# Performance work log

Hardware: AMD Instinct MI355X
Metric: run time of the kernel (lower is better)

## Reference

```python
import jax, jax.numpy as jnp
import numpy as np

B, M, IN, H = 4096, 16, 512, 512


def _linear_params(key, out_dim, in_dim):
    kw, kb = jax.random.split(key)
    s = 1.0 / np.sqrt(in_dim)
    W = jax.random.uniform(kw, (out_dim, in_dim), jnp.float32, -s, s)
    b = jax.random.uniform(kb, (out_dim,), jnp.float32, -s, s)
    return W, b


def setup_inputs() -> dict:
    key = jax.random.key(0)
    ks = jax.random.split(key, 15)
    inp = {
        "input": jax.random.normal(ks[0], (B, IN), jnp.float32),
        "h0": jax.random.normal(ks[1], (B, H), jnp.float32),
        "c0": jax.random.normal(ks[2], (B, H), jnp.float32),
        "all_c_b_e_w": jax.random.normal(ks[3], (B, M, H), jnp.float32),
        "all_num_word": jax.random.randint(ks[4], (B,), 0, M + 1, jnp.int32),
    }
    names = ["ii", "hi", "if_", "hf", "ig", "hg", "io", "ho", "lx", "lc"]
    in_dims = [IN, H, IN, H, IN, H, IN, H, IN, H]
    for n, d, k in zip(names, in_dims, ks[5:15]):
        W, b = _linear_params(k, H, d)
        inp["W_" + n] = W
        inp["b_" + n] = b
    return inp


def _lin(x, W, b):
    return x @ W.T + b


def reference(input, h0, c0, all_c_b_e_w, all_num_word,
              W_ii, b_ii, W_hi, b_hi, W_if_, b_if_, W_hf, b_hf,
              W_ig, b_ig, W_hg, b_hg, W_io, b_io, W_ho, b_ho,
              W_lx, b_lx, W_lc, b_lc):
    i = jax.nn.sigmoid(_lin(input, W_ii, b_ii) + _lin(h0, W_hi, b_hi))   # [B,H]
    f = jax.nn.sigmoid(_lin(input, W_if_, b_if_) + _lin(h0, W_hf, b_hf))  # computed but unused, as in original
    g = jnp.tanh(_lin(input, W_ig, b_ig) + _lin(h0, W_hg, b_hg))         # [B,H]
    o = jax.nn.sigmoid(_lin(input, W_io, b_io) + _lin(h0, W_ho, b_ho))   # [B,H]

    # lattice word-cell gates, vectorized over the ragged word dim with a mask
    lx = _lin(input, W_lx, b_lx)                 # [B,H]
    lc = _lin(all_c_b_e_w, W_lc, b_lc)           # [B,M,H]
    i_b = jax.nn.sigmoid(lx[:, None, :] + lc)    # [B,M,H]
    mask = (jnp.arange(M)[None, :] < all_num_word[:, None])  # [B,M]
    exp_b = jnp.exp(i_b) * mask[:, :, None].astype(i_b.dtype)  # [B,M,H]
    exp_i = jnp.exp(i)                                         # [B,H]
    denom = exp_i + jnp.sum(exp_b, axis=1)                     # [B,H]
    c_words = jnp.sum((exp_b / denom[:, None, :]) * all_c_b_e_w, axis=1)
    c_lat = c_words + (exp_i / denom) * g
    c = jnp.where((all_num_word > 0)[:, None], c_lat, g)       # num_word==0 -> c=g
    h1 = o * jnp.tanh(c)
    return (h1, c)
```

## Files before the change

### kernel.cpp

```cpp
#include <hip/hip_runtime.h>
#include <hip/hip_bf16.h>
#include <stdint.h>


typedef __attribute__((ext_vector_type(8))) short short8;
typedef __attribute__((ext_vector_type(4))) float f32x4;
typedef __attribute__((ext_vector_type(4))) unsigned short us4;

__device__ __forceinline__ unsigned short f2bf(float f) {
  union { float f; unsigned u; } v; v.f = f;
  return (unsigned short)((v.u + 0x7fffu + ((v.u >> 16) & 1u)) >> 16);
}
__device__ __forceinline__ unsigned short f2bf_h(float f) {
  __hip_bfloat16 h = __float2bfloat16(f);
  return *reinterpret_cast<unsigned short*>(&h);
}
__device__ __forceinline__ float bf2f(unsigned short u) {
  return __uint_as_float((unsigned)u << 16);
}
__device__ __forceinline__ float sigmoidf_(float x) {
  return 1.f / (1.f + __expf(-x));
}
__device__ __forceinline__ float fast_tanh(float x) {
  float e = __expf(-2.f * fmaxf(x, -30.f));
  return (1.f - e) / (1.f + e);
}

__global__ void k_cvt_all(const float* __restrict__ x, const float* __restrict__ h,
                          const float* __restrict__ Wii, const float* __restrict__ Wig,
                          const float* __restrict__ Wio, const float* __restrict__ Wlx,
                          const float* __restrict__ Whi, const float* __restrict__ Whg,
                          const float* __restrict__ Who, const float* __restrict__ Wlcf,
                          unsigned short* __restrict__ XH, unsigned short* __restrict__ Wcat,
                          unsigned short* __restrict__ Wlc) {
  const int bb = blockIdx.x;
  const int tid = threadIdx.x;
  us4 o;
  if (bb < 4096) {
    const int t = bb * 256 + tid;
    const int b = t >> 8;
    const int col = (t & 255) * 4;
    const float* src = (col < 512) ? (x + (size_t)b * 512 + col)
                                   : (h + (size_t)b * 512 + (col - 512));
    f32x4 v = *(const f32x4*)src;
    o[0] = f2bf(v[0]); o[1] = f2bf(v[1]); o[2] = f2bf(v[2]); o[3] = f2bf(v[3]);
    *(us4*)(XH + (size_t)t * 4) = o;
  } else if (bb < 6144) {
    const int t = (bb - 4096) * 256 + tid;
    const int row = t >> 8;
    const int col = (t & 255) * 4;
    const int sec = row >> 9, r = row & 511;
    if (col < 512) {
      const float* W = sec == 0 ? Wii : sec == 1 ? Wig : sec == 2 ? Wio : Wlx;
      f32x4 v = *(const f32x4*)(W + (size_t)r * 512 + col);
      o[0] = f2bf(v[0]); o[1] = f2bf(v[1]); o[2] = f2bf(v[2]); o[3] = f2bf(v[3]);
    } else if (sec < 3) {
      const float* W = sec == 0 ? Whi : sec == 1 ? Whg : Who;
      f32x4 v = *(const f32x4*)(W + (size_t)r * 512 + (col - 512));
      o[0] = f2bf(v[0]); o[1] = f2bf(v[1]); o[2] = f2bf(v[2]); o[3] = f2bf(v[3]);
    } else {
      o[0] = 0; o[1] = 0; o[2] = 0; o[3] = 0;
    }
    *(us4*)(Wcat + (size_t)t * 4) = o;
  } else {
    const int t = (bb - 6144) * 256 + tid;
    f32x4 v = *(const f32x4*)(Wlcf + (size_t)t * 4);
    o[0] = f2bf(v[0]); o[1] = f2bf(v[1]); o[2] = f2bf(v[2]); o[3] = f2bf(v[3]);
    *(us4*)(Wlc + (size_t)t * 4) = o;
  }
}

__global__ __launch_bounds__(256) void k_gemm0(
    const unsigned short* __restrict__ A, const unsigned short* __restrict__ Bm,
    unsigned short* __restrict__ C, int Ndim, int Kdim, int nbx) {
  __shared__ unsigned short As[2][128 * 64];
  __shared__ unsigned short Bs[2][128 * 64];
  const int tid = threadIdx.x;
  const int lane = tid & 63, wid = tid >> 6;
  const int wr = wid >> 1, wc = wid & 1;
  const int l15 = lane & 15, lhi = lane >> 4;

  const int chunk = gridDim.x >> 3;
  const int bid = (blockIdx.x & 7) * chunk + (blockIdx.x >> 3);
  const int brow = bid / nbx, bcol = bid % nbx;
  const int m0 = brow * 128, n0 = bcol * 128;

  f32x4 acc[4][4];
#pragma unroll
  for (int i = 0; i < 4; ++i)
#pragma unroll
    for (int j = 0; j < 4; ++j) acc[i][j] = (f32x4){0.f, 0.f, 0.f, 0.f};

  const int cb0 = wid * 64;
  auto stage = [&](int buf, int k0) {
#pragma unroll
    for (int q = 0; q < 4; ++q) {
      const int cb = q * 256 + cb0;
      const int chunkid = cb + lane;
      const int row = chunkid >> 3, slot = chunkid & 7;
      const int kk = k0 + ((slot ^ (row & 7)) << 3);
      __builtin_amdgcn_global_load_lds(
          (const __attribute__((address_space(1))) unsigned int*)(A + (size_t)(m0 + row) * Kdim + kk),
          (__attribute__((address_space(3))) unsigned int*)(As[buf] + cb * 8), 16, 0, 0);
      __builtin_amdgcn_global_load_lds(
          (const __attribute__((address_space(1))) unsigned int*)(Bm + (size_t)(n0 + row) * Kdim + kk),
          (__attribute__((address_space(3))) unsigned int*)(Bs[buf] + cb * 8), 16, 0, 0);
    }
  };

  const int nt = Kdim >> 6;
  stage(0, 0);
  __syncthreads();

  const int swz = (lane & 7) << 4;
  for (int t = 0; t < nt; ++t) {
    const int cur = t & 1;
    if (t + 1 < nt) stage(cur ^ 1, (t + 1) << 6);
    const char* Ab = (const char*)As[cur];
    const char* Bb = (const char*)Bs[cur];
#pragma unroll
    for (int s = 0; s < 2; ++s) {
      short8 av[4], bv[4];
#pragma unroll
      for (int mi = 0; mi < 4; ++mi) {
        const int row = wr * 64 + mi * 16 + l15;
        av[mi] = *(const short8*)(Ab + row * 128 + ((s * 64 + lhi * 16) ^ swz));
      }
#pragma unroll
      for (int ni = 0; ni < 4; ++ni) {
        const int row = wc * 64 + ni * 16 + l15;
        bv[ni] = *(const short8*)(Bb + row * 128 + ((s * 64 + lhi * 16) ^ swz));
      }
#pragma unroll
      for (int mi = 0; mi < 4; ++mi)
#pragma unroll
        for (int ni = 0; ni < 4; ++ni)
          acc[mi][ni] = __builtin_amdgcn_mfma_f32_16x16x32_bf16(av[mi], bv[ni], acc[mi][ni], 0, 0, 0);
    }
    __syncthreads();
  }

#pragma unroll
  for (int mi = 0; mi < 4; ++mi) {
    const int gr = m0 + wr * 64 + mi * 16 + lhi * 4;
#pragma unroll
    for (int ni = 0; ni < 4; ++ni) {
      const int gc = n0 + wc * 64 + ni * 16 + l15;
#pragma unroll
      for (int j = 0; j < 4; ++j)
        C[(size_t)(gr + j) * Ndim + gc] = f2bf(acc[mi][ni][j]);
    }
  }
}

__global__ __launch_bounds__(512) void k_latg(
    const float* __restrict__ Af,
    const unsigned short* __restrict__ Bm,
    const int* __restrict__ num_word,
    unsigned short* __restrict__ lcb) {
  __shared__ unsigned short As[2][256 * 32];
  __shared__ unsigned short Bs[2][256 * 32];
  const int tid = threadIdx.x;
  const int lane = tid & 63, wid = tid >> 6;
  const int wrow = wid >> 2, wcol = wid & 3;
  const int l15 = lane & 15, lhi = lane >> 4;

  const int chunk = gridDim.x >> 3;
  const int bid = (blockIdx.x & 7) * chunk + (blockIdx.x >> 3);
  const int brow = bid >> 1, bcol = bid & 1;
  const int m0 = brow * 256, n0 = bcol * 256;

  f32x4 acc[8][4];
#pragma unroll
  for (int i = 0; i < 8; ++i)
#pragma unroll
    for (int j = 0; j < 4; ++j) acc[i][j] = (f32x4){0.f, 0.f, 0.f, 0.f};

  f32x4 SA[2][2], SB[2][2];

  auto loadA = [&](f32x4 (&dst)[2][2], int k0) {
#pragma unroll
    for (int q = 0; q < 2; ++q) {
      const int c = q * 512 + tid;
      const int row = c >> 2, s = c & 3;
      const float* p = Af + (size_t)(m0 + row) * 512 + k0 + s * 8;
      dst[q][0] = *(const f32x4*)p;
      dst[q][1] = *(const f32x4*)(p + 4);
    }
  };
  auto writeA = [&](int buf, f32x4 (&src)[2][2]) {
#pragma unroll
    for (int q = 0; q < 2; ++q) {
      const int c = q * 512 + tid;
      const int row = c >> 2, s = c & 3;
      const int pr = row >> 1;
      const int phys = (s + ((row & 1) << 2)) ^ (pr & 7);
      short8 v;
      v[0] = (short)f2bf_h(src[q][0][0]); v[1] = (short)f2bf_h(src[q][0][1]);
      v[2] = (short)f2bf_h(src[q][0][2]); v[3] = (short)f2bf_h(src[q][0][3]);
      v[4] = (short)f2bf_h(src[q][1][0]); v[5] = (short)f2bf_h(src[q][1][1]);
      v[6] = (short)f2bf_h(src[q][1][2]); v[7] = (short)f2bf_h(src[q][1][3]);
      *(short8*)((char*)As[buf] + pr * 128 + phys * 16) = v;
    }
  };
  auto stageB = [&](int buf, int k0) {
#pragma unroll
    for (int q = 0; q < 2; ++q) {
      const int cb = q * 512 + wid * 64;
      const int c = cb + lane;
      const int pr = c >> 3, phys = c & 7;
      const int gi = phys ^ (pr & 7);
      const int row = pr * 2 + (gi >> 2);
      const int kk = k0 + ((gi & 3) << 3);
      __builtin_amdgcn_global_load_lds(
          (const __attribute__((address_space(1))) unsigned int*)(Bm + (size_t)(n0 + row) * 512 + kk),
          (__attribute__((address_space(3))) unsigned int*)(Bs[buf] + cb * 8), 16, 0, 0);
    }
  };

  auto compute = [&](int buf) {
    const char* Ab = (const char*)As[buf];
    const char* Bb = (const char*)Bs[buf];
    short8 av[8], bv[4];
#pragma unroll
    for (int mi = 0; mi < 8; ++mi) {
      const int row = wrow * 128 + mi * 16 + l15;
      const int pr = row >> 1;
      av[mi] = *(const short8*)(Ab + pr * 128 +
                (((lhi + ((row & 1) << 2)) ^ (pr & 7)) << 4));
    }
#pragma unroll
    for (int ni = 0; ni < 4; ++ni) {
      const int row = wcol * 64 + ni * 16 + l15;
      const int pr = row >> 1;
      bv[ni] = *(const short8*)(Bb + pr * 128 +
                (((lhi + ((row & 1) << 2)) ^ (pr & 7)) << 4));
    }
    __builtin_amdgcn_s_setprio(1);
#pragma unroll
    for (int mi = 0; mi < 8; ++mi)
#pragma unroll
      for (int ni = 0; ni < 4; ++ni)
        acc[mi][ni] = __builtin_amdgcn_mfma_f32_16x16x32_bf16(av[mi], bv[ni], acc[mi][ni], 0, 0, 0);
    __builtin_amdgcn_s_setprio(0);
  };

  loadA(SA, 0);
  loadA(SB, 32);
  stageB(0, 0);
  writeA(0, SA);
  __syncthreads();

#pragma unroll 1
  for (int t = 0; t < 16; t += 2) {
    if (t + 2 < 16) loadA(SA, (t + 2) << 5);
    if (t + 1 < 16) stageB(1, (t + 1) << 5);
    compute(0);
    if (t + 1 < 16) writeA(1, SB);
    __syncthreads();
    if (t + 3 < 16) loadA(SB, (t + 3) << 5);
    if (t + 2 < 16) stageB(0, (t + 2) << 5);
    compute(1);
    if (t + 2 < 16) writeA(0, SA);
    __syncthreads();
  }

#pragma unroll
  for (int mi = 0; mi < 8; ++mi) {
    const int rbase = m0 + wrow * 128 + mi * 16;
    const int nw = num_word[rbase >> 4];
    const int gr = rbase + lhi * 4;
#pragma unroll
    for (int ni = 0; ni < 4; ++ni) {
      const int gc = n0 + wcol * 64 + ni * 16 + l15;
#pragma unroll
      for (int j = 0; j < 4; ++j)
        if (lhi * 4 + j < nw)
          lcb[(size_t)(gr + j) * 512 + gc] = f2bf(acc[mi][ni][j]);
    }
  }
}

__global__ __launch_bounds__(512) void k_epi(
    const unsigned short* __restrict__ lc,
    const float* __restrict__ all_c,
    const unsigned short* __restrict__ C1u,
    const int* __restrict__ num_word,
    const float* __restrict__ b_ii, const float* __restrict__ b_hi,
    const float* __restrict__ b_ig, const float* __restrict__ b_hg,
    const float* __restrict__ b_io, const float* __restrict__ b_ho,
    const float* __restrict__ b_lx, const float* __restrict__ b_lc,
    float* __restrict__ outH, float* __restrict__ outC) {
  const int b = blockIdx.x;
  const int hc = threadIdx.x;
  const int nw = num_word[b];
  const size_t base = (size_t)b * 2048;

  const float pre = bf2f(C1u[base + 1536 + hc]) + b_lx[hc] + b_lc[hc];
  const unsigned short* lcp = lc + ((size_t)b * 16) * 512 + hc;
  const float* wp = all_c + ((size_t)b * 16) * 512 + hc;

  float se = 0.f, sew = 0.f;
#pragma unroll 4
  for (int m = 0; m < nw; ++m) {
    const float ib = sigmoidf_(pre + bf2f(lcp[(size_t)m * 512]));
    const float e = __expf(ib);
    se += e;
    sew += e * wp[(size_t)m * 512];
  }

  const float ig = sigmoidf_(bf2f(C1u[base + hc]) + b_ii[hc] + b_hi[hc]);
  const float g  = fast_tanh(bf2f(C1u[base + 512 + hc]) + b_ig[hc] + b_hg[hc]);
  const float og = sigmoidf_(bf2f(C1u[base + 1024 + hc]) + b_io[hc] + b_ho[hc]);
  const float ei = __expf(ig);
  const float denom = ei + se;
  const float cc = (sew + ei * g) / denom;
  outH[(size_t)b * 512 + hc] = og * fast_tanh(cc);
  outC[(size_t)b * 512 + hc] = cc;
}

extern "C" void kernel_launch(void* const* d_in, const int* in_sizes, int n_in,
                              void* d_out, int out_size, void* d_ws, size_t ws_size,
                              hipStream_t stream) {
  const float* input    = (const float*)d_in[0];
  const float* h0       = (const float*)d_in[1];
  const float* all_c    = (const float*)d_in[3];
  const int*   num_word = (const int*)d_in[4];
  const float* W_ii = (const float*)d_in[5];  const float* b_ii = (const float*)d_in[6];
  const float* W_hi = (const float*)d_in[7];  const float* b_hi = (const float*)d_in[8];
  const float* W_ig = (const float*)d_in[13]; const float* b_ig = (const float*)d_in[14];
  const float* W_hg = (const float*)d_in[15]; const float* b_hg = (const float*)d_in[16];
  const float* W_io = (const float*)d_in[17]; const float* b_io = (const float*)d_in[18];
  const float* W_ho = (const float*)d_in[19]; const float* b_ho = (const float*)d_in[20];
  const float* W_lx = (const float*)d_in[21]; const float* b_lx = (const float*)d_in[22];
  const float* W_lc = (const float*)d_in[23]; const float* b_lc = (const float*)d_in[24];

  char* ws = (char*)d_ws;
  unsigned short* XH   = (unsigned short*)(ws);
  unsigned short* Wcat = (unsigned short*)(ws + 8388608);
  unsigned short* Wlc  = (unsigned short*)(ws + 12582912);
  unsigned short* C1u  = (unsigned short*)(ws + 13107200);
  unsigned short* lc   = (unsigned short*)(ws + 29884416);

  float* outH = (float*)d_out;
  float* outC = outH + (size_t)4096 * 512;

  k_cvt_all<<<6400, 256, 0, stream>>>(input, h0, W_ii, W_ig, W_io, W_lx,
                                      W_hi, W_hg, W_ho, W_lc, XH, Wcat, Wlc);

  k_gemm0<<<512, 256, 0, stream>>>(XH, Wcat, C1u, 2048, 1024, 16);

  k_latg<<<512, 512, 0, stream>>>(all_c, Wlc, num_word, lc);

  k_epi<<<4096, 512, 0, stream>>>(lc, all_c, C1u, num_word,
      b_ii, b_hi, b_ig, b_hg, b_io, b_ho, b_lx, b_lc, outH, outC);
}
```

Before: 112.2 us.

## Compact ragged word rows via prefix scan before lattice GEMM

Adds a single-block scan kernel that computes per-batch offsets and a row map of only the valid (batch, word) rows. The lattice GEMM now gathers A rows through that map and blocks beyond the compacted row count exit early, so padded word rows are never loaded or multiplied. The epilogue reads lc at compacted offsets. This costs an extra serial launch and gathered (less contiguous) A loads, in exchange for skipping roughly half of the lattice GEMM work when num_word is uniform over 0..16.

```diff
diff --git a/kernel.cpp b/kernel.cpp
--- a/kernel.cpp
+++ b/kernel.cpp
@@ -70,6 +70,49 @@
   }
 }
 
+__global__ __launch_bounds__(1024) void k_scan(const int* __restrict__ nwp,
+                                               int* __restrict__ off,
+                                               int* __restrict__ row_map) {
+  const int tid = threadIdx.x;
+  const int lane = tid & 63, wid = tid >> 6;
+  __shared__ int wsum[16];
+  __shared__ int stotal;
+  int n[4];
+  int s = 0;
+#pragma unroll
+  for (int i = 0; i < 4; ++i) {
+    int v = nwp[tid * 4 + i];
+    v = min(max(v, 0), 16);
+    n[i] = v; s += v;
+  }
+  int sc = s;
+  for (int d = 1; d < 64; d <<= 1) {
+    int t = __shfl_up(sc, d, 64);
+    if (lane >= d) sc += t;
+  }
+  if (lane == 63) wsum[wid] = sc;
+  __syncthreads();
+  if (tid == 0) {
+    int acc = 0;
+    for (int w = 0; w < 16; ++w) { int t = wsum[w]; wsum[w] = acc; acc += t; }
+    stotal = acc;
+  }
+  __syncthreads();
+  int excl = wsum[wid] + sc - s;
+#pragma unroll
+  for (int i = 0; i < 4; ++i) {
+    const int b = tid * 4 + i;
+    off[b] = excl;
+    for (int m = 0; m < n[i]; ++m) row_map[excl + m] = b * 16 + m;
+    excl += n[i];
+  }
+  __syncthreads();
+  const int total = stotal;
+  if (tid == 0) off[4096] = total;
+  const int padded = (total + 255) & ~255;
+  for (int idx = total + tid; idx < padded; idx += 1024) row_map[idx] = 0;
+}
+
 __global__ __launch_bounds__(256) void k_gemm0(
     const unsigned short* __restrict__ A, const unsigned short* __restrict__ Bm,
     unsigned short* __restrict__ C, int Ndim, int Kdim, int nbx) {
@@ -156,7 +199,8 @@
 __global__ __launch_bounds__(512) void k_latg(
     const float* __restrict__ Af,
     const unsigned short* __restrict__ Bm,
-    const int* __restrict__ num_word,
+    const int* __restrict__ row_map,
+    const int* __restrict__ totalp,
     unsigned short* __restrict__ lcb) {
   __shared__ unsigned short As[2][256 * 32];
   __shared__ unsigned short Bs[2][256 * 32];
@@ -165,11 +209,17 @@
   const int wrow = wid >> 2, wcol = wid & 3;
   const int l15 = lane & 15, lhi = lane >> 4;
 
+  const int total = totalp[0];
+  const int nact = ((total + 255) >> 8) << 1;
   const int chunk = gridDim.x >> 3;
   const int bid = (blockIdx.x & 7) * chunk + (blockIdx.x >> 3);
+  if (bid >= nact) return;
   const int brow = bid >> 1, bcol = bid & 1;
   const int m0 = brow * 256, n0 = bcol * 256;
 
+  int orow0 = row_map[m0 + (tid >> 2)];
+  int orow1 = row_map[m0 + 128 + (tid >> 2)];
+
   f32x4 acc[8][4];
 #pragma unroll
   for (int i = 0; i < 8; ++i)
@@ -181,9 +231,9 @@
   auto loadA = [&](f32x4 (&dst)[2][2], int k0) {
 #pragma unroll
     for (int q = 0; q < 2; ++q) {
-      const int c = q * 512 + tid;
-      const int row = c >> 2, s = c & 3;
-      const float* p = Af + (size_t)(m0 + row) * 512 + k0 + s * 8;
+      const int orow = q ? orow1 : orow0;
+      const int s = tid & 3;
+      const float* p = Af + (size_t)orow * 512 + k0 + s * 8;
       dst[q][0] = *(const f32x4*)p;
       dst[q][1] = *(const f32x4*)(p + 4);
     }
@@ -267,16 +317,16 @@
 
 #pragma unroll
   for (int mi = 0; mi < 8; ++mi) {
-    const int rbase = m0 + wrow * 128 + mi * 16;
-    const int nw = num_word[rbase >> 4];
-    const int gr = rbase + lhi * 4;
+    const int rbase = m0 + wrow * 128 + mi * 16 + lhi * 4;
 #pragma unroll
     for (int ni = 0; ni < 4; ++ni) {
       const int gc = n0 + wcol * 64 + ni * 16 + l15;
 #pragma unroll
-      for (int j = 0; j < 4; ++j)
-        if (lhi * 4 + j < nw)
-          lcb[(size_t)(gr + j) * 512 + gc] = f2bf(acc[mi][ni][j]);
+      for (int j = 0; j < 4; ++j) {
+        const int rc = rbase + j;
+        if (rc < total)
+          lcb[(size_t)rc * 512 + gc] = f2bf(acc[mi][ni][j]);
+      }
     }
   }
 }
@@ -286,6 +336,7 @@
     const float* __restrict__ all_c,
     const unsigned short* __restrict__ C1u,
     const int* __restrict__ num_word,
+    const int* __restrict__ off,
     const float* __restrict__ b_ii, const float* __restrict__ b_hi,
     const float* __restrict__ b_ig, const float* __restrict__ b_hg,
     const float* __restrict__ b_io, const float* __restrict__ b_ho,
@@ -297,7 +348,7 @@
   const size_t base = (size_t)b * 2048;
 
   const float pre = bf2f(C1u[base + 1536 + hc]) + b_lx[hc] + b_lc[hc];
-  const unsigned short* lcp = lc + ((size_t)b * 16) * 512 + hc;
+  const unsigned short* lcp = lc + (size_t)off[b] * 512 + hc;
   const float* wp = all_c + ((size_t)b * 16) * 512 + hc;
 
   float se = 0.f, sew = 0.f;
@@ -341,6 +392,8 @@
   unsigned short* Wlc  = (unsigned short*)(ws + 12582912);
   unsigned short* C1u  = (unsigned short*)(ws + 13107200);
   unsigned short* lc   = (unsigned short*)(ws + 29884416);
+  int*            off  = (int*)(ws + 96993280);
+  int*            rmap = (int*)(ws + 97026048);
 
   float* outH = (float*)d_out;
   float* outC = outH + (size_t)4096 * 512;
@@ -348,10 +401,12 @@
   k_cvt_all<<<6400, 256, 0, stream>>>(input, h0, W_ii, W_ig, W_io, W_lx,
                                       W_hi, W_hg, W_ho, W_lc, XH, Wcat, Wlc);
 
+  k_scan<<<1, 1024, 0, stream>>>(num_word, off, rmap);
+
   k_gemm0<<<512, 256, 0, stream>>>(XH, Wcat, C1u, 2048, 1024, 16);
 
-  k_latg<<<512, 512, 0, stream>>>(all_c, Wlc, num_word, lc);
-
-  k_epi<<<4096, 512, 0, stream>>>(lc, all_c, C1u, num_word,
+  k_latg<<<512, 512, 0, stream>>>(all_c, Wlc, rmap, off + 4096, lc);
+
+  k_epi<<<4096, 512, 0, stream>>>(lc, all_c, C1u, num_word, off,
       b_ii, b_hi, b_ig, b_hg, b_io, b_ho, b_lx, b_lc, outH, outC);
 }
```

Result: slower. 116.4 us (+3.7%).
